# Performance work log

Measured on AMD Instinct MI355X. Metric: run time of the kernel, lower is better.

Reference implementation:

```python
import jax, jax.numpy as jnp
import numpy as np

N = 8192
IN_DIM = 256
HID = 512
NUM_CLASSES = 256
AVG_DEG = 32


def setup_inputs() -> dict:
    key = jax.random.key(0)
    k_a, k_x, k_w1, k_w2 = jax.random.split(key, 4)
    # Binary adjacency with avg degree ~AVG_DEG (entries are exactly 1.0, matching
    # A.nonzero() edge extraction with implicit unit edge weights).
    A = (jax.random.uniform(k_a, (N, N)) < (AVG_DEG / N)).astype(jnp.float32)
    x = jax.random.normal(k_x, (N, IN_DIM), dtype=jnp.float32)
    # GCNConv params: glorot-ish weights, zero bias.
    W1 = jax.random.normal(k_w1, (IN_DIM, HID), dtype=jnp.float32) / np.sqrt(IN_DIM)
    b1 = jnp.zeros((HID,), dtype=jnp.float32)
    W2 = jax.random.normal(k_w2, (HID, NUM_CLASSES), dtype=jnp.float32) / np.sqrt(HID)
    b2 = jnp.zeros((NUM_CLASSES,), dtype=jnp.float32)
    sigmoid_param = jnp.array([10.0], dtype=jnp.float32)
    return {"A": A, "x": x, "W1": W1, "b1": b1, "W2": W2, "b2": b2,
            "sigmoid_param": sigmoid_param}


def _gcn_propagate(A, deg_inv_sqrt, h):
    # PyG GCNConv aggregation with self-loops, without materializing A + I:
    # out_j = d_j^{-1/2} * sum_i A_ij d_i^{-1/2} h_i  +  d_j^{-1} h_j
    m = deg_inv_sqrt[:, None] * h              # [N, d]
    agg = A.T @ m                              # messages flow row -> col
    return deg_inv_sqrt[:, None] * agg + (deg_inv_sqrt[:, None] ** 2) * h


def reference(A, x, W1, b1, W2, b2, sigmoid_param):
    # Degree from column sums of (A + I) — matches gcn_norm's scatter on col.
    deg = jnp.sum(A, axis=0) + 1.0             # [N], >= 1 thanks to self-loop
    deg_inv_sqrt = jax.lax.rsqrt(deg)
    skip_x = x                                  # nn.Identity skip connection
    # GCNConv 1: linear then normalized aggregation, then bias; ReLU.
    h = _gcn_propagate(A, deg_inv_sqrt, x @ W1) + b1
    h = jax.nn.relu(h)
    # GCNConv 2.
    h = _gcn_propagate(A, deg_inv_sqrt, h @ W2) + b2
    # Skip add + scaled sigmoid (original casts to double; kept float32 here).
    return jax.nn.sigmoid(sigmoid_param * (h + skip_x))
```

## Files before the change

kernel.cpp:

```cpp
#include <hip/hip_runtime.h>
#include <hip/hip_bf16.h>

#define N_NODES 8192
#define IN_DIM  256
#define HID     512
#define NCLS    256
#define CAP     128
#define PXK     (IN_DIM + 8)
#define LDSK    (HID + 8)

typedef __attribute__((ext_vector_type(8))) __bf16 bf16x8;
typedef __attribute__((ext_vector_type(4))) float  floatx4;

static __device__ __forceinline__ float bf2f(ushort u) {
    union { float f; unsigned int i; } v; v.i = ((unsigned int)u) << 16; return v.f;
}
static __device__ __forceinline__ ushort f2bf(float f) {
    __hip_bfloat16 b = __float2bfloat16(f);
    return *reinterpret_cast<ushort*>(&b);
}
static __device__ __forceinline__ void bfpair(unsigned int u, float& lo, float& hi) {
    union { float f; unsigned int i; } a, b;
    a.i = u << 16; b.i = u & 0xFFFF0000u;
    lo = a.f; hi = b.f;
}

static __device__ __forceinline__ void gcn_gather256(const ushort* __restrict__ tab,
                                                     const int* __restrict__ col_idx,
                                                     const int* __restrict__ col_cnt,
                                                     int j, int d,
                                                     float& a0, float& a1, float& a2, float& a3) {
    const int cntraw = col_cnt[j];
    const int cnt = min(cntraw, CAP);
    const float dj = rsqrtf((float)cntraw + 1.0f);
    {
        const uint2 sv = *reinterpret_cast<const uint2*>(tab + (size_t)j * 256 + d);
        float f0, f1, f2, f3;
        bfpair(sv.x, f0, f1); bfpair(sv.y, f2, f3);
        a0 = dj * f0; a1 = dj * f1; a2 = dj * f2; a3 = dj * f3;
    }
    const int* __restrict__ lst = col_idx + (size_t)j * CAP;
    int e = 0;
    for (; e + 8 <= cnt; e += 8) {
        uint2 rv[8]; float we[8];
#pragma unroll
        for (int q = 0; q < 8; ++q) {
            const int i = lst[e + q];
            rv[q] = *reinterpret_cast<const uint2*>(tab + (size_t)i * 256 + d);
            we[q] = rsqrtf((float)col_cnt[i] + 1.0f);
        }
#pragma unroll
        for (int q = 0; q < 8; ++q) {
            float f0, f1, f2, f3;
            bfpair(rv[q].x, f0, f1); bfpair(rv[q].y, f2, f3);
            a0 += we[q] * f0; a1 += we[q] * f1; a2 += we[q] * f2; a3 += we[q] * f3;
        }
    }
    for (; e < cnt; ++e) {
        const int i = lst[e];
        const uint2 rv = *reinterpret_cast<const uint2*>(tab + (size_t)i * 256 + d);
        const float we = rsqrtf((float)col_cnt[i] + 1.0f);
        float f0, f1, f2, f3;
        bfpair(rv.x, f0, f1); bfpair(rv.y, f2, f3);
        a0 += we * f0; a1 += we * f1; a2 += we * f2; a3 += we * f3;
    }
    a0 *= dj; a1 *= dj; a2 *= dj; a3 *= dj;
}

__global__ __launch_bounds__(256) void scan_conv(const float* __restrict__ A,
                                                 const float* __restrict__ x,
                                                 const float* __restrict__ W1,
                                                 const float* __restrict__ W2,
                                                 int* __restrict__ col_cnt,
                                                 int* __restrict__ col_idx,
                                                 ushort* __restrict__ xb,
                                                 ushort* __restrict__ W1Th, ushort* __restrict__ W1Tl,
                                                 ushort* __restrict__ W2Th, ushort* __restrict__ W2Tl) {
    if (blockIdx.y >= 256) {
        const int idx = ((blockIdx.y - 256) * 8 + blockIdx.x) * 256 + threadIdx.x;
        {
            const int i = idx * 4;
            const floatx4 v = *reinterpret_cast<const floatx4*>(x + i);
            *reinterpret_cast<ushort4*>(xb + i) = ushort4{f2bf(v.x), f2bf(v.y), f2bf(v.z), f2bf(v.w)};
        }
        if (idx < IN_DIM * HID) {
            {
                const int k = idx / HID, n = idx % HID;
                const float v = W1[idx]; const ushort h = f2bf(v);
                W1Th[(size_t)n * IN_DIM + k] = h;
                W1Tl[(size_t)n * IN_DIM + k] = f2bf(v - bf2f(h));
            }
            {
                const int k = idx / NCLS, n = idx % NCLS;
                const float v = W2[idx]; const ushort h = f2bf(v);
                W2Th[(size_t)n * HID + k] = h;
                W2Tl[(size_t)n * HID + k] = f2bf(v - bf2f(h));
            }
        }
        return;
    }
    const int jbase = (blockIdx.x * 256 + threadIdx.x) * 4;
    const int i0 = blockIdx.y * 32;
    const float* base = A + (size_t)i0 * N_NODES + jbase;
    floatx4 v0 = __builtin_nontemporal_load(reinterpret_cast<const floatx4*>(base));
    floatx4 v1 = __builtin_nontemporal_load(reinterpret_cast<const floatx4*>(base + N_NODES));
#define PROC(v, irow) do { \
    if ((v).x != 0.0f) { int q = atomicAdd(&col_cnt[jbase + 0], 1); if (q < CAP) col_idx[(size_t)(jbase + 0) * CAP + q] = (irow); } \
    if ((v).y != 0.0f) { int q = atomicAdd(&col_cnt[jbase + 1], 1); if (q < CAP) col_idx[(size_t)(jbase + 1) * CAP + q] = (irow); } \
    if ((v).z != 0.0f) { int q = atomicAdd(&col_cnt[jbase + 2], 1); if (q < CAP) col_idx[(size_t)(jbase + 2) * CAP + q] = (irow); } \
    if ((v).w != 0.0f) { int q = atomicAdd(&col_cnt[jbase + 3], 1); if (q < CAP) col_idx[(size_t)(jbase + 3) * CAP + q] = (irow); } \
} while (0)
    for (int ii = 0; ii < 32; ii += 2) {
        floatx4 n0 = {}, n1 = {};
        if (ii + 2 < 32) {
            n0 = __builtin_nontemporal_load(reinterpret_cast<const floatx4*>(base + (size_t)(ii + 2) * N_NODES));
            n1 = __builtin_nontemporal_load(reinterpret_cast<const floatx4*>(base + (size_t)(ii + 3) * N_NODES));
        }
        PROC(v0, i0 + ii);
        PROC(v1, i0 + ii + 1);
        v0 = n0; v1 = n1;
    }
#undef PROC
}

__global__ __launch_bounds__(256) void gemm12_fused(const ushort* __restrict__ xb,
                                                    const int* __restrict__ col_idx,
                                                    const int* __restrict__ col_cnt,
                                                    const ushort* __restrict__ B1h,
                                                    const ushort* __restrict__ B1l,
                                                    const float* __restrict__ b1,
                                                    const ushort* __restrict__ B2h,
                                                    const ushort* __restrict__ B2l,
                                                    ushort* __restrict__ g2b) {
    __shared__ __align__(16) ushort pxs[32 * PXK];
    __shared__ __align__(16) ushort hs[32 * LDSK];
    const int tid = threadIdx.x;
    const int lane = tid & 63, wave = tid >> 6;
    const int l16 = lane & 15, quad = lane >> 4;
    const int m_blk = blockIdx.x * 32;

    {
        const int d = lane * 4;
#pragma unroll 1
        for (int s = 0; s < 8; ++s) {
            const int jl = wave * 8 + s;
            const int j = __builtin_amdgcn_readfirstlane(m_blk + jl);
            float a0, a1, a2, a3;
            gcn_gather256(xb, col_idx, col_cnt, j, d, a0, a1, a2, a3);
            *reinterpret_cast<ushort4*>(&pxs[jl * PXK + d]) =
                ushort4{f2bf(a0), f2bf(a1), f2bf(a2), f2bf(a3)};
        }
    }
    __syncthreads();

    {
        const int n_base = wave * 128;
        floatx4 acc[2][8] = {};
#pragma unroll 1
        for (int k0 = 0; k0 < IN_DIM; k0 += 32) {
            const int kf = k0 + quad * 8;
            bf16x8 a[2], bh[8], bl[8];
#pragma unroll
            for (int t = 0; t < 2; ++t)
                a[t] = *reinterpret_cast<const bf16x8*>(pxs + (size_t)(t * 16 + l16) * PXK + kf);
#pragma unroll
            for (int t = 0; t < 8; ++t) {
                const size_t bo = (size_t)(n_base + t * 16 + l16) * IN_DIM + kf;
                bh[t] = *reinterpret_cast<const bf16x8*>(B1h + bo);
                bl[t] = *reinterpret_cast<const bf16x8*>(B1l + bo);
            }
#pragma unroll
            for (int tm = 0; tm < 2; ++tm)
#pragma unroll
                for (int tn = 0; tn < 8; ++tn) {
                    acc[tm][tn] = __builtin_amdgcn_mfma_f32_16x16x32_bf16(a[tm], bl[tn], acc[tm][tn], 0, 0, 0);
                    acc[tm][tn] = __builtin_amdgcn_mfma_f32_16x16x32_bf16(a[tm], bh[tn], acc[tm][tn], 0, 0, 0);
                }
        }
#pragma unroll
        for (int tn = 0; tn < 8; ++tn) {
            const int col = n_base + tn * 16 + l16;
            const float bv = b1[col];
#pragma unroll
            for (int tm = 0; tm < 2; ++tm)
#pragma unroll
                for (int r = 0; r < 4; ++r) {
                    const int row = tm * 16 + quad * 4 + r;
                    hs[row * LDSK + col] = f2bf(fmaxf(acc[tm][tn][r] + bv, 0.0f));
                }
        }
    }
    __syncthreads();

    {
        const int n_base = wave * 64;
        floatx4 acc[2][4] = {};
#pragma unroll 2
        for (int k0 = 0; k0 < HID; k0 += 32) {
            const int kf = k0 + quad * 8;
            bf16x8 a[2], bh[4], bl[4];
#pragma unroll
            for (int t = 0; t < 2; ++t)
                a[t] = *reinterpret_cast<const bf16x8*>(hs + (size_t)(t * 16 + l16) * LDSK + kf);
#pragma unroll
            for (int t = 0; t < 4; ++t) {
                const size_t bo = (size_t)(n_base + t * 16 + l16) * HID + kf;
                bh[t] = *reinterpret_cast<const bf16x8*>(B2h + bo);
                bl[t] = *reinterpret_cast<const bf16x8*>(B2l + bo);
            }
#pragma unroll
            for (int tm = 0; tm < 2; ++tm)
#pragma unroll
                for (int tn = 0; tn < 4; ++tn) {
                    acc[tm][tn] = __builtin_amdgcn_mfma_f32_16x16x32_bf16(a[tm], bl[tn], acc[tm][tn], 0, 0, 0);
                    acc[tm][tn] = __builtin_amdgcn_mfma_f32_16x16x32_bf16(a[tm], bh[tn], acc[tm][tn], 0, 0, 0);
                }
        }
#pragma unroll
        for (int tm = 0; tm < 2; ++tm)
#pragma unroll
            for (int tn = 0; tn < 4; ++tn)
#pragma unroll
                for (int r = 0; r < 4; ++r)
                    g2b[(size_t)(m_blk + tm * 16 + quad * 4 + r) * NCLS + (n_base + tn * 16 + l16)] =
                        f2bf(acc[tm][tn][r]);
    }
}

__global__ __launch_bounds__(256) void agg_out(const ushort* __restrict__ g2b,
                                               const int* __restrict__ col_idx,
                                               const int* __restrict__ col_cnt,
                                               const float* __restrict__ b2,
                                               const float* __restrict__ x,
                                               const float* __restrict__ sp_p,
                                               float* __restrict__ out) {
    const int j = __builtin_amdgcn_readfirstlane(blockIdx.x * 4 + (threadIdx.x >> 6));
    const int d = (threadIdx.x & 63) * 4;
    float a0, a1, a2, a3;
    gcn_gather256(g2b, col_idx, col_cnt, j, d, a0, a1, a2, a3);
    const float sp = sp_p[0];
    const floatx4 bv = *reinterpret_cast<const floatx4*>(b2 + d);
    const floatx4 xv = __builtin_nontemporal_load(
        reinterpret_cast<const floatx4*>(x + (size_t)j * NCLS + d));
    floatx4 o;
    o.x = 1.0f / (1.0f + __expf(-sp * (a0 + bv.x + xv.x)));
    o.y = 1.0f / (1.0f + __expf(-sp * (a1 + bv.y + xv.y)));
    o.z = 1.0f / (1.0f + __expf(-sp * (a2 + bv.z + xv.z)));
    o.w = 1.0f / (1.0f + __expf(-sp * (a3 + bv.w + xv.w)));
    __builtin_nontemporal_store(o, reinterpret_cast<floatx4*>(out + (size_t)j * NCLS + d));
}

extern "C" void kernel_launch(void* const* d_in, const int* in_sizes, int n_in,
                              void* d_out, int out_size, void* d_ws, size_t ws_size,
                              hipStream_t stream) {
    const float* A  = (const float*)d_in[0];
    const float* x  = (const float*)d_in[1];
    const float* W1 = (const float*)d_in[2];
    const float* b1 = (const float*)d_in[3];
    const float* W2 = (const float*)d_in[4];
    const float* b2 = (const float*)d_in[5];
    const float* sp = (const float*)d_in[6];
    float* out = (float*)d_out;

    char* ws = (char*)d_ws;
    size_t off = 0;
    auto alloc = [&](size_t bytes) {
        void* p = ws + off;
        off = (off + bytes + 255) & ~(size_t)255;
        return p;
    };
    int*    col_cnt = (int*)   alloc((size_t)N_NODES * 4);
    int*    col_idx = (int*)   alloc((size_t)N_NODES * CAP * 4);
    ushort* xb      = (ushort*)alloc((size_t)N_NODES * IN_DIM * 2);
    ushort* W1Th    = (ushort*)alloc((size_t)HID * IN_DIM * 2);
    ushort* W1Tl    = (ushort*)alloc((size_t)HID * IN_DIM * 2);
    ushort* W2Th    = (ushort*)alloc((size_t)NCLS * HID * 2);
    ushort* W2Tl    = (ushort*)alloc((size_t)NCLS * HID * 2);
    ushort* g2b     = (ushort*)alloc((size_t)N_NODES * NCLS * 2);

    (void)hipMemsetAsync(col_cnt, 0, (size_t)N_NODES * 4, stream);

    scan_conv<<<dim3(8, 512), 256, 0, stream>>>(
        A, x, W1, W2, col_cnt, col_idx, xb, W1Th, W1Tl, W2Th, W2Tl);

    gemm12_fused<<<N_NODES / 32, 256, 0, stream>>>(
        xb, col_idx, col_cnt, W1Th, W1Tl, b1, W2Th, W2Tl, g2b);

    agg_out<<<N_NODES / 4, 256, 0, stream>>>(g2b, col_idx, col_cnt, b2, x, sp, out);
}
```

Before: 444.1 us.

## Split first-layer gather into separate agg_x kernel and simplify adjacency scan

The neighbor aggregation of x, previously done inside the fused GEMM kernel into shared memory, moves to its own agg_x kernel that writes a bf16 aggregated-feature buffer to global memory. The GEMM then reads its A operand straight from that buffer. The aim is more parallelism for the latency-bound gather (4 nodes per block across 2048 blocks instead of 256 blocks) and lighter GEMM blocks. The cost is an extra kernel launch and a global write and read of the intermediate. The adjacency scan also drops its manual two-row software prefetch in favor of a plain per-row loop.

```diff
diff --git a/kernel.cpp b/kernel.cpp
--- a/kernel.cpp
+++ b/kernel.cpp
@@ -6,7 +6,6 @@
 #define HID     512
 #define NCLS    256
 #define CAP     128
-#define PXK     (IN_DIM + 8)
 #define LDSK    (HID + 8)
 
 typedef __attribute__((ext_vector_type(8))) __bf16 bf16x8;
@@ -101,57 +100,41 @@
     }
     const int jbase = (blockIdx.x * 256 + threadIdx.x) * 4;
     const int i0 = blockIdx.y * 32;
-    const float* base = A + (size_t)i0 * N_NODES + jbase;
-    floatx4 v0 = __builtin_nontemporal_load(reinterpret_cast<const floatx4*>(base));
-    floatx4 v1 = __builtin_nontemporal_load(reinterpret_cast<const floatx4*>(base + N_NODES));
-#define PROC(v, irow) do { \
-    if ((v).x != 0.0f) { int q = atomicAdd(&col_cnt[jbase + 0], 1); if (q < CAP) col_idx[(size_t)(jbase + 0) * CAP + q] = (irow); } \
-    if ((v).y != 0.0f) { int q = atomicAdd(&col_cnt[jbase + 1], 1); if (q < CAP) col_idx[(size_t)(jbase + 1) * CAP + q] = (irow); } \
-    if ((v).z != 0.0f) { int q = atomicAdd(&col_cnt[jbase + 2], 1); if (q < CAP) col_idx[(size_t)(jbase + 2) * CAP + q] = (irow); } \
-    if ((v).w != 0.0f) { int q = atomicAdd(&col_cnt[jbase + 3], 1); if (q < CAP) col_idx[(size_t)(jbase + 3) * CAP + q] = (irow); } \
-} while (0)
-    for (int ii = 0; ii < 32; ii += 2) {
-        floatx4 n0 = {}, n1 = {};
-        if (ii + 2 < 32) {
-            n0 = __builtin_nontemporal_load(reinterpret_cast<const floatx4*>(base + (size_t)(ii + 2) * N_NODES));
-            n1 = __builtin_nontemporal_load(reinterpret_cast<const floatx4*>(base + (size_t)(ii + 3) * N_NODES));
-        }
-        PROC(v0, i0 + ii);
-        PROC(v1, i0 + ii + 1);
-        v0 = n0; v1 = n1;
-    }
-#undef PROC
-}
-
-__global__ __launch_bounds__(256) void gemm12_fused(const ushort* __restrict__ xb,
-                                                    const int* __restrict__ col_idx,
-                                                    const int* __restrict__ col_cnt,
+    for (int ii = 0; ii < 32; ++ii) {
+        const int i = i0 + ii;
+        const floatx4* p = reinterpret_cast<const floatx4*>(A + (size_t)i * N_NODES + jbase);
+        floatx4 v = __builtin_nontemporal_load(p);
+        if (v.x != 0.0f) { int q = atomicAdd(&col_cnt[jbase + 0], 1); if (q < CAP) col_idx[(size_t)(jbase + 0) * CAP + q] = i; }
+        if (v.y != 0.0f) { int q = atomicAdd(&col_cnt[jbase + 1], 1); if (q < CAP) col_idx[(size_t)(jbase + 1) * CAP + q] = i; }
+        if (v.z != 0.0f) { int q = atomicAdd(&col_cnt[jbase + 2], 1); if (q < CAP) col_idx[(size_t)(jbase + 2) * CAP + q] = i; }
+        if (v.w != 0.0f) { int q = atomicAdd(&col_cnt[jbase + 3], 1); if (q < CAP) col_idx[(size_t)(jbase + 3) * CAP + q] = i; }
+    }
+}
+
+__global__ __launch_bounds__(256) void agg_x(const ushort* __restrict__ xb,
+                                             const int* __restrict__ col_idx,
+                                             const int* __restrict__ col_cnt,
+                                             ushort* __restrict__ px) {
+    const int j = __builtin_amdgcn_readfirstlane(blockIdx.x * 4 + (threadIdx.x >> 6));
+    const int d = (threadIdx.x & 63) * 4;
+    float a0, a1, a2, a3;
+    gcn_gather256(xb, col_idx, col_cnt, j, d, a0, a1, a2, a3);
+    *reinterpret_cast<ushort4*>(px + (size_t)j * IN_DIM + d) =
+        ushort4{f2bf(a0), f2bf(a1), f2bf(a2), f2bf(a3)};
+}
+
+__global__ __launch_bounds__(256) void gemm12_fused(const ushort* __restrict__ A,
                                                     const ushort* __restrict__ B1h,
                                                     const ushort* __restrict__ B1l,
                                                     const float* __restrict__ b1,
                                                     const ushort* __restrict__ B2h,
                                                     const ushort* __restrict__ B2l,
                                                     ushort* __restrict__ g2b) {
-    __shared__ __align__(16) ushort pxs[32 * PXK];
     __shared__ __align__(16) ushort hs[32 * LDSK];
     const int tid = threadIdx.x;
     const int lane = tid & 63, wave = tid >> 6;
     const int l16 = lane & 15, quad = lane >> 4;
     const int m_blk = blockIdx.x * 32;
-
-    {
-        const int d = lane * 4;
-#pragma unroll 1
-        for (int s = 0; s < 8; ++s) {
-            const int jl = wave * 8 + s;
-            const int j = __builtin_amdgcn_readfirstlane(m_blk + jl);
-            float a0, a1, a2, a3;
-            gcn_gather256(xb, col_idx, col_cnt, j, d, a0, a1, a2, a3);
-            *reinterpret_cast<ushort4*>(&pxs[jl * PXK + d]) =
-                ushort4{f2bf(a0), f2bf(a1), f2bf(a2), f2bf(a3)};
-        }
-    }
-    __syncthreads();
 
     {
         const int n_base = wave * 128;
@@ -162,7 +145,7 @@
             bf16x8 a[2], bh[8], bl[8];
 #pragma unroll
             for (int t = 0; t < 2; ++t)
-                a[t] = *reinterpret_cast<const bf16x8*>(pxs + (size_t)(t * 16 + l16) * PXK + kf);
+                a[t] = *reinterpret_cast<const bf16x8*>(A + (size_t)(m_blk + t * 16 + l16) * IN_DIM + kf);
 #pragma unroll
             for (int t = 0; t < 8; ++t) {
                 const size_t bo = (size_t)(n_base + t * 16 + l16) * IN_DIM + kf;
@@ -272,6 +255,7 @@
     int*    col_cnt = (int*)   alloc((size_t)N_NODES * 4);
     int*    col_idx = (int*)   alloc((size_t)N_NODES * CAP * 4);
     ushort* xb      = (ushort*)alloc((size_t)N_NODES * IN_DIM * 2);
+    ushort* px      = (ushort*)alloc((size_t)N_NODES * IN_DIM * 2);
     ushort* W1Th    = (ushort*)alloc((size_t)HID * IN_DIM * 2);
     ushort* W1Tl    = (ushort*)alloc((size_t)HID * IN_DIM * 2);
     ushort* W2Th    = (ushort*)alloc((size_t)NCLS * HID * 2);
@@ -283,8 +267,9 @@
     scan_conv<<<dim3(8, 512), 256, 0, stream>>>(
         A, x, W1, W2, col_cnt, col_idx, xb, W1Th, W1Tl, W2Th, W2Tl);
 
+    agg_x<<<N_NODES / 4, 256, 0, stream>>>(xb, col_idx, col_cnt, px);
     gemm12_fused<<<N_NODES / 32, 256, 0, stream>>>(
-        xb, col_idx, col_cnt, W1Th, W1Tl, b1, W2Th, W2Tl, g2b);
+        px, W1Th, W1Tl, b1, W2Th, W2Tl, g2b);
 
     agg_out<<<N_NODES / 4, 256, 0, stream>>>(g2b, col_idx, col_cnt, b2, x, sp, out);
 }
```

Measured after the change: 428.8 us. 1.04x faster.
